# Kernel tuning notes

Hardware: AMD Instinct MI355X
Metric: run time of the kernel (lower is better)

The kernel has to match this reference:

```python
import jax, jax.numpy as jnp
import numpy as np

IN_F = 256
OUT_F = 256
H = 4
HD = OUT_F // H  # 64
N = 20000
E = 160000
B = 1
LN_EPS = 1e-5
NEG_SLOPE = 0.2


def setup_inputs() -> dict:
    key = jax.random.key(0)
    k1, k2, k3, k4 = jax.random.split(key, 4)
    node_features = jax.random.normal(k1, (B, N, IN_F), dtype=jnp.float32)
    edge_index = jax.random.randint(k2, (2, E), 0, N, dtype=jnp.int64)
    # per-head linear weights, stacked: [H, IN_F, HD]
    W = jax.random.normal(k3, (H, IN_F, HD), dtype=jnp.float32) / np.sqrt(IN_F)
    # per-head attention vectors on concat([src, dst]): [H, 2*HD]
    a = jax.random.normal(k4, (H, 2 * HD), dtype=jnp.float32) / np.sqrt(2 * HD)
    gamma = jnp.ones((OUT_F,), dtype=jnp.float32)
    beta = jnp.zeros((OUT_F,), dtype=jnp.float32)
    return {"node_features": node_features, "edge_index": edge_index,
            "W": W, "a": a, "gamma": gamma, "beta": beta}


def reference(node_features, edge_index, W, a, gamma, beta):
    src_idx, dst_idx = edge_index[0], edge_index[1]
    # per-head linear transform: [B, H, N, HD]
    t = jnp.einsum('bnf,hfd->bhnd', node_features, W)
    # gather edge endpoints: [B, H, E, HD]
    src = t[:, :, src_idx, :]
    dst = t[:, :, dst_idx, :]
    # attention score = a . concat(src, dst), split a into halves
    scores = (jnp.einsum('bhed,hd->bhe', src, a[:, :HD]) +
              jnp.einsum('bhed,hd->bhe', dst, a[:, HD:]))
    scores = jnp.where(scores >= 0, scores, NEG_SLOPE * scores)
    # NOTE: faithful to the original — softmax over ALL edges (dim=-1), not per-destination
    w = jax.nn.softmax(scores, axis=-1)  # [B, H, E]
    # scatter-add weighted src features into destination nodes
    agg = jnp.zeros_like(t).at[:, :, dst_idx, :].add(w[..., None] * src)  # [B, H, N, HD]
    # concat heads (head-major, matching torch.cat over head_outputs)
    out = agg.transpose(0, 2, 1, 3).reshape(B, N, OUT_F)
    # LayerNorm
    mean = out.mean(-1, keepdims=True)
    var = out.var(-1, keepdims=True)
    out = (out - mean) / jnp.sqrt(var + LN_EPS) * gamma + beta
    return out
```

## Files before the change

### kernel.cpp

```cpp
#include <hip/hip_runtime.h>

#define IN_F   256
#define OUT_F  256
#define NHEAD  4
#define HD     64
#define NN     20000
#define NE     160000
#define LN_EPS 1e-5f
#define SLOPE  0.2f
#define BUCKET 64
#define SE_BLOCKS 256

typedef __attribute__((ext_vector_type(8))) short short8;
typedef __attribute__((ext_vector_type(4))) float f32x4;

__device__ __forceinline__ unsigned short rne_bf16(float f) {
  unsigned u = __float_as_uint(f);
  u += 0x7FFFu + ((u >> 16) & 1u);
  return (unsigned short)(u >> 16);
}
__device__ __forceinline__ float bf2f(unsigned short u) {
  return __uint_as_float((unsigned)u << 16);
}
__device__ __forceinline__ unsigned pk2(float lo, float hi) {
  return (unsigned)rne_bf16(lo) | ((unsigned)rne_bf16(hi) << 16);
}

__global__ __launch_bounds__(256) void conv_w(const float* __restrict__ W,
                                              unsigned short* __restrict__ Wt,
                                              int* __restrict__ deg) {
  int i = blockIdx.x * 256 + threadIdx.x;
  if (i < NN) deg[i] = 0;
  if (i < 16384) {
    int fq  = i & 63;
    int col = i >> 6;
    int h = col >> 6, d = col & 63;
    const float* src = W + ((size_t)h * IN_F + fq * 4) * HD + d;
    ushort4 o;
    o.x = rne_bf16(src[0]);
    o.y = rne_bf16(src[64]);
    o.z = rne_bf16(src[128]);
    o.w = rne_bf16(src[192]);
    *reinterpret_cast<ushort4*>(Wt + (size_t)col * IN_F + fq * 4) = o;
  }
}

__global__ __launch_bounds__(256) void gemm_mfma(const float* __restrict__ X,
                                                 const unsigned short* __restrict__ Wt,
                                                 const float* __restrict__ a,
                                                 unsigned short* __restrict__ Tb,
                                                 float* __restrict__ asrc,
                                                 float* __restrict__ adst) {
  __shared__ unsigned Alds[64 * 32];
  __shared__ unsigned Blds[256 * 32];
  const int tid  = threadIdx.x;
  const int lane = tid & 63;
  const int wid  = tid >> 6;
  const int row0 = blockIdx.x * 64;

  f32x4 acc[4][4];
  #pragma unroll
  for (int r = 0; r < 4; ++r)
    #pragma unroll
    for (int c = 0; c < 4; ++c) acc[r][c] = (f32x4){0.f, 0.f, 0.f, 0.f};

  const int ar = tid >> 2;
  const int aq = tid & 3;
  const int s0 = (aq * 2) ^ (ar & 7);
  const int s1 = (aq * 2 + 1) ^ (ar & 7);
  const bool aok = (row0 + ar) < NN;
  const float* xrow = X + (size_t)(row0 + ar) * IN_F + aq * 16;

  for (int kt = 0; kt < 4; ++kt) {
    const int k0 = kt * 64;
    if (kt) __syncthreads();
    float4 x0 = {0,0,0,0}, x1 = {0,0,0,0}, x2 = {0,0,0,0}, x3 = {0,0,0,0};
    if (aok) {
      const float4* xp = reinterpret_cast<const float4*>(xrow + k0);
      x0 = xp[0]; x1 = xp[1]; x2 = xp[2]; x3 = xp[3];
    }
    uint4 U0 = {pk2(x0.x,x0.y), pk2(x0.z,x0.w), pk2(x1.x,x1.y), pk2(x1.z,x1.w)};
    uint4 U1 = {pk2(x2.x,x2.y), pk2(x2.z,x2.w), pk2(x3.x,x3.y), pk2(x3.z,x3.w)};
    *reinterpret_cast<uint4*>(&Alds[ar * 32 + s0 * 4]) = U0;
    *reinterpret_cast<uint4*>(&Alds[ar * 32 + s1 * 4]) = U1;
    #pragma unroll
    for (int i = 0; i < 8; ++i) {
      int c   = wid * 8 + i;
      int col = c * 8 + (lane >> 3);
      int kch = (lane & 7) ^ (col & 7);
      const unsigned short* src = Wt + (size_t)col * IN_F + k0 + kch * 8;
      __builtin_amdgcn_global_load_lds(
          (const __attribute__((address_space(1))) void*)src,
          (__attribute__((address_space(3))) void*)((char*)Blds + c * 1024),
          16, 0, 0);
    }
    __syncthreads();
    const int g = lane >> 4;
    #pragma unroll
    for (int kf = 0; kf < 2; ++kf) {
      short8 afr[4], bfr[4];
      #pragma unroll
      for (int r = 0; r < 4; ++r) {
        int row  = 16 * r + (lane & 15);
        int slot = (4 * kf + g) ^ (row & 7);
        afr[r] = *reinterpret_cast<const short8*>(&Alds[row * 32 + slot * 4]);
      }
      #pragma unroll
      for (int c = 0; c < 4; ++c) {
        int col  = wid * 64 + 16 * c + (lane & 15);
        int slot = (4 * kf + g) ^ (col & 7);
        bfr[c] = *reinterpret_cast<const short8*>(&Blds[col * 32 + slot * 4]);
      }
      #pragma unroll
      for (int r = 0; r < 4; ++r)
        #pragma unroll
        for (int c = 0; c < 4; ++c)
          acc[r][c] = __builtin_amdgcn_mfma_f32_16x16x32_bf16(afr[r], bfr[c], acc[r][c], 0, 0, 0);
    }
  }

  const int g  = lane >> 4;
  const int lc = lane & 15;
  float as_[4], ad_[4];
  #pragma unroll
  for (int fc = 0; fc < 4; ++fc) {
    as_[fc] = a[wid * 128 + fc * 16 + lc];
    ad_[fc] = a[wid * 128 + 64 + fc * 16 + lc];
  }
  #pragma unroll
  for (int r = 0; r < 4; ++r) {
    #pragma unroll
    for (int reg = 0; reg < 4; ++reg) {
      int row = row0 + 16 * r + g * 4 + reg;
      float ps = 0.f, pd = 0.f;
      if (row < NN) {
        #pragma unroll
        for (int fc = 0; fc < 4; ++fc) {
          float v = acc[r][fc][reg];
          ps = fmaf(v, as_[fc], ps);
          pd = fmaf(v, ad_[fc], pd);
          Tb[(size_t)row * OUT_F + wid * 64 + fc * 16 + lc] = rne_bf16(v);
        }
      }
      #pragma unroll
      for (int off = 1; off < 16; off <<= 1) {
        ps += __shfl_xor(ps, off, 64);
        pd += __shfl_xor(pd, off, 64);
      }
      if (lc == 0 && row < NN) {
        asrc[row * 4 + wid] = ps;
        adst[row * 4 + wid] = pd;
      }
    }
  }
}

__global__ __launch_bounds__(256) void score_exp_fill(const int* __restrict__ ei,
                                                      const float* __restrict__ asrc,
                                                      const float* __restrict__ adst,
                                                      float* __restrict__ partials,
                                                      int* __restrict__ deg,
                                                      int* __restrict__ srcs,
                                                      float4* __restrict__ wbuck) {
  __shared__ float red[4][4];
  const int tid  = threadIdx.x;
  const int lane = tid & 63;
  const int wid  = tid >> 6;
  float acc[4] = {0.f, 0.f, 0.f, 0.f};

  for (int e = blockIdx.x * 256 + tid; e < NE; e += SE_BLOCKS * 256) {
    int s = ei[e], t = ei[NE + e];
    float4 av = reinterpret_cast<const float4*>(asrc)[s];
    float4 dv = reinterpret_cast<const float4*>(adst)[t];
    float sc[4] = {av.x + dv.x, av.y + dv.y, av.z + dv.z, av.w + dv.w};
    float ex[4];
    #pragma unroll
    for (int h = 0; h < 4; ++h) {
      sc[h] = sc[h] >= 0.f ? sc[h] : SLOPE * sc[h];
      ex[h] = expf(sc[h]);
      acc[h] += ex[h];
    }
    int pos = atomicAdd(&deg[t], 1);
    srcs[t * BUCKET + pos]  = s;
    wbuck[t * BUCKET + pos] = make_float4(ex[0], ex[1], ex[2], ex[3]);
  }
  #pragma unroll
  for (int off = 1; off < 64; off <<= 1) {
    #pragma unroll
    for (int h = 0; h < 4; ++h) acc[h] += __shfl_xor(acc[h], off, 64);
  }
  if (lane == 0) {
    #pragma unroll
    for (int h = 0; h < 4; ++h) red[wid][h] = acc[h];
  }
  __syncthreads();
  if (tid < 4)
    partials[blockIdx.x * 4 + tid] = red[0][tid] + red[1][tid] + red[2][tid] + red[3][tid];
}

__global__ __launch_bounds__(256) void agg_ln_kernel(const int* __restrict__ deg,
                                                     const int* __restrict__ srcs,
                                                     const float* __restrict__ wbuck,
                                                     const float* __restrict__ partials,
                                                     const unsigned short* __restrict__ Tb,
                                                     const float* __restrict__ gamma,
                                                     const float* __restrict__ beta,
                                                     float* __restrict__ out) {
  __shared__ float red[256];
  const int tid  = threadIdx.x;
  const int lane = tid & 63;
  const int n    = blockIdx.x * 4 + (tid >> 6);
  const int h    = lane >> 4;

  float psum = partials[tid] + partials[tid + 256] + partials[tid + 512] + partials[tid + 768];

  int d = deg[n];
  const int*   bs = srcs  + (size_t)n * BUCKET;
  const float* bw = wbuck + (size_t)n * BUCKET * 4;
  const ushort4* T4 = reinterpret_cast<const ushort4*>(Tb);
  float4 acc = make_float4(0.f, 0.f, 0.f, 0.f);

  int p = 0;
  for (; p + 4 <= d; p += 4) {
    int s0 = bs[p], s1 = bs[p + 1], s2 = bs[p + 2], s3 = bs[p + 3];
    float w0 = bw[(p + 0) * 4 + h], w1 = bw[(p + 1) * 4 + h];
    float w2 = bw[(p + 2) * 4 + h], w3 = bw[(p + 3) * 4 + h];
    ushort4 v0 = T4[(size_t)s0 * 64 + lane];
    ushort4 v1 = T4[(size_t)s1 * 64 + lane];
    ushort4 v2 = T4[(size_t)s2 * 64 + lane];
    ushort4 v3 = T4[(size_t)s3 * 64 + lane];
    acc.x = fmaf(w3, bf2f(v3.x), fmaf(w2, bf2f(v2.x), fmaf(w1, bf2f(v1.x), fmaf(w0, bf2f(v0.x), acc.x))));
    acc.y = fmaf(w3, bf2f(v3.y), fmaf(w2, bf2f(v2.y), fmaf(w1, bf2f(v1.y), fmaf(w0, bf2f(v0.y), acc.y))));
    acc.z = fmaf(w3, bf2f(v3.z), fmaf(w2, bf2f(v2.z), fmaf(w1, bf2f(v1.z), fmaf(w0, bf2f(v0.z), acc.z))));
    acc.w = fmaf(w3, bf2f(v3.w), fmaf(w2, bf2f(v2.w), fmaf(w1, bf2f(v1.w), fmaf(w0, bf2f(v0.w), acc.w))));
  }
  for (; p < d; ++p) {
    int s0 = bs[p];
    float w0 = bw[p * 4 + h];
    ushort4 v0 = T4[(size_t)s0 * 64 + lane];
    acc.x = fmaf(w0, bf2f(v0.x), acc.x);
    acc.y = fmaf(w0, bf2f(v0.y), acc.y);
    acc.z = fmaf(w0, bf2f(v0.z), acc.z);
    acc.w = fmaf(w0, bf2f(v0.w), acc.w);
  }

  red[tid] = psum;
  __syncthreads();
  if (tid < 128) red[tid] += red[tid + 128];
  __syncthreads();
  if (tid < 64) red[tid] += red[tid + 64];
  __syncthreads();
  if (tid < 32) red[tid] += red[tid + 32];
  __syncthreads();
  if (tid < 16) red[tid] += red[tid + 16];
  __syncthreads();
  if (tid < 8) red[tid] += red[tid + 8];
  __syncthreads();
  if (tid < 4) red[tid] += red[tid + 4];
  __syncthreads();
  float rs = 1.0f / red[h];

  acc.x *= rs; acc.y *= rs; acc.z *= rs; acc.w *= rs;

  float s = acc.x + acc.y + acc.z + acc.w;
  float q = acc.x * acc.x + acc.y * acc.y + acc.z * acc.z + acc.w * acc.w;
  #pragma unroll
  for (int off = 1; off < 64; off <<= 1) {
    s += __shfl_xor(s, off, 64);
    q += __shfl_xor(q, off, 64);
  }
  float mean = s * (1.f / 256.f);
  float var  = q * (1.f / 256.f) - mean * mean;
  float rstd = rsqrtf(var + LN_EPS);
  float4 g = reinterpret_cast<const float4*>(gamma)[lane];
  float4 b = reinterpret_cast<const float4*>(beta)[lane];
  float4 o;
  o.x = (acc.x - mean) * rstd * g.x + b.x;
  o.y = (acc.y - mean) * rstd * g.y + b.y;
  o.z = (acc.z - mean) * rstd * g.z + b.z;
  o.w = (acc.w - mean) * rstd * g.w + b.w;
  reinterpret_cast<float4*>(out)[(size_t)n * 64 + lane] = o;
}

extern "C" void kernel_launch(void* const* d_in, const int* in_sizes, int n_in,
                              void* d_out, int out_size, void* d_ws, size_t ws_size,
                              hipStream_t stream) {
  const float* X     = (const float*)d_in[0];
  const int*   ei    = (const int*)d_in[1];
  const float* W     = (const float*)d_in[2];
  const float* a     = (const float*)d_in[3];
  const float* gamma = (const float*)d_in[4];
  const float* beta  = (const float*)d_in[5];
  float* out = (float*)d_out;

  float* ws = (float*)d_ws;
  const size_t OFF_DEG   = 16;
  const size_t OFF_PART  = OFF_DEG + NN;
  const size_t OFF_SRCS  = OFF_PART + 1024;
  const size_t OFF_WB    = OFF_SRCS + (size_t)NN * BUCKET;
  const size_t OFF_WT    = OFF_WB + (size_t)NN * BUCKET * 4;
  const size_t OFF_T     = OFF_WT + 32768;
  const size_t OFF_ASRC  = OFF_T + (size_t)NN * 128;
  const size_t OFF_ADST  = OFF_ASRC + NN * 4;

  int*            deg      = (int*)(ws + OFF_DEG);
  float*          partials = ws + OFF_PART;
  int*            srcs     = (int*)(ws + OFF_SRCS);
  float4*         wbuck    = (float4*)(ws + OFF_WB);
  unsigned short* Wt       = (unsigned short*)(ws + OFF_WT);
  unsigned short* Tb       = (unsigned short*)(ws + OFF_T);
  float*          asrc     = ws + OFF_ASRC;
  float*          adst     = ws + OFF_ADST;

  conv_w<<<80, 256, 0, stream>>>(W, Wt, deg);
  gemm_mfma<<<(NN + 63) / 64, 256, 0, stream>>>(X, Wt, a, Tb, asrc, adst);
  score_exp_fill<<<SE_BLOCKS, 256, 0, stream>>>(ei, asrc, adst, partials, deg, srcs,
                                                (float4*)wbuck);
  agg_ln_kernel<<<NN / 4, 256, 0, stream>>>(deg, srcs, (const float*)wbuck, partials,
                                            Tb, gamma, beta, out);
}
```

Baseline: 60.22 us.

## Pack edge buckets into int4 with bf16 weights and broadcast via shuffles

Merges the separate source-index and float4 weight buckets into one int4 record per edge, with the exp weights packed as bf16. The aggregation wave loads its whole bucket once (one slot per lane) and broadcasts source and weight with shuffles. Gathers are unrolled in chunks of 8/4/2/1 so more loads are in flight. This cuts bucket memory traffic and dependent scalar loads, at the cost of bf16 rounding on the attention weights and extra shuffle instructions.

```diff
diff --git a/kernel.cpp b/kernel.cpp
--- a/kernel.cpp
+++ b/kernel.cpp
@@ -160,8 +160,7 @@
                                                       const float* __restrict__ adst,
                                                       float* __restrict__ partials,
                                                       int* __restrict__ deg,
-                                                      int* __restrict__ srcs,
-                                                      float4* __restrict__ wbuck) {
+                                                      int4* __restrict__ bucket) {
   __shared__ float red[4][4];
   const int tid  = threadIdx.x;
   const int lane = tid & 63;
@@ -181,8 +180,8 @@
       acc[h] += ex[h];
     }
     int pos = atomicAdd(&deg[t], 1);
-    srcs[t * BUCKET + pos]  = s;
-    wbuck[t * BUCKET + pos] = make_float4(ex[0], ex[1], ex[2], ex[3]);
+    bucket[(size_t)t * BUCKET + pos] =
+        make_int4(s, (int)pk2(ex[0], ex[1]), (int)pk2(ex[2], ex[3]), 0);
   }
   #pragma unroll
   for (int off = 1; off < 64; off <<= 1) {
@@ -199,8 +198,7 @@
 }
 
 __global__ __launch_bounds__(256) void agg_ln_kernel(const int* __restrict__ deg,
-                                                     const int* __restrict__ srcs,
-                                                     const float* __restrict__ wbuck,
+                                                     const int4* __restrict__ bucket,
                                                      const float* __restrict__ partials,
                                                      const unsigned short* __restrict__ Tb,
                                                      const float* __restrict__ gamma,
@@ -215,34 +213,43 @@
   float psum = partials[tid] + partials[tid + 256] + partials[tid + 512] + partials[tid + 768];
 
   int d = deg[n];
-  const int*   bs = srcs  + (size_t)n * BUCKET;
-  const float* bw = wbuck + (size_t)n * BUCKET * 4;
+  int4 bv = bucket[(size_t)n * BUCKET + lane];
   const ushort4* T4 = reinterpret_cast<const ushort4*>(Tb);
   float4 acc = make_float4(0.f, 0.f, 0.f, 0.f);
 
+  #define SLOT_SW(pp, sv, wv)                                              \
+    {                                                                      \
+      sv = __shfl(bv.x, (pp), 64);                                         \
+      int _wl = __shfl(bv.y, (pp), 64);                                    \
+      int _wh = __shfl(bv.z, (pp), 64);                                    \
+      int _wd = (lane < 32) ? _wl : _wh;                                   \
+      wv = bf2f((unsigned short)((h & 1) ? ((unsigned)_wd >> 16)           \
+                                         : ((unsigned)_wd & 0xffffu)));    \
+    }
+  #define GATHER_CHUNK(CN)                                                 \
+    {                                                                      \
+      int sL[CN]; float wL[CN]; ushort4 vL[CN];                            \
+      _Pragma("unroll")                                                    \
+      for (int j = 0; j < CN; ++j) SLOT_SW(p + j, sL[j], wL[j]);           \
+      _Pragma("unroll")                                                    \
+      for (int j = 0; j < CN; ++j) vL[j] = T4[(size_t)sL[j] * 64 + lane];  \
+      _Pragma("unroll")                                                    \
+      for (int j = 0; j < CN; ++j) {                                       \
+        acc.x = fmaf(wL[j], bf2f(vL[j].x), acc.x);                         \
+        acc.y = fmaf(wL[j], bf2f(vL[j].y), acc.y);                         \
+        acc.z = fmaf(wL[j], bf2f(vL[j].z), acc.z);                         \
+        acc.w = fmaf(wL[j], bf2f(vL[j].w), acc.w);                         \
+      }                                                                    \
+      p += CN;                                                             \
+    }
+
   int p = 0;
-  for (; p + 4 <= d; p += 4) {
-    int s0 = bs[p], s1 = bs[p + 1], s2 = bs[p + 2], s3 = bs[p + 3];
-    float w0 = bw[(p + 0) * 4 + h], w1 = bw[(p + 1) * 4 + h];
-    float w2 = bw[(p + 2) * 4 + h], w3 = bw[(p + 3) * 4 + h];
-    ushort4 v0 = T4[(size_t)s0 * 64 + lane];
-    ushort4 v1 = T4[(size_t)s1 * 64 + lane];
-    ushort4 v2 = T4[(size_t)s2 * 64 + lane];
-    ushort4 v3 = T4[(size_t)s3 * 64 + lane];
-    acc.x = fmaf(w3, bf2f(v3.x), fmaf(w2, bf2f(v2.x), fmaf(w1, bf2f(v1.x), fmaf(w0, bf2f(v0.x), acc.x))));
-    acc.y = fmaf(w3, bf2f(v3.y), fmaf(w2, bf2f(v2.y), fmaf(w1, bf2f(v1.y), fmaf(w0, bf2f(v0.y), acc.y))));
-    acc.z = fmaf(w3, bf2f(v3.z), fmaf(w2, bf2f(v2.z), fmaf(w1, bf2f(v1.z), fmaf(w0, bf2f(v0.z), acc.z))));
-    acc.w = fmaf(w3, bf2f(v3.w), fmaf(w2, bf2f(v2.w), fmaf(w1, bf2f(v1.w), fmaf(w0, bf2f(v0.w), acc.w))));
-  }
-  for (; p < d; ++p) {
-    int s0 = bs[p];
-    float w0 = bw[p * 4 + h];
-    ushort4 v0 = T4[(size_t)s0 * 64 + lane];
-    acc.x = fmaf(w0, bf2f(v0.x), acc.x);
-    acc.y = fmaf(w0, bf2f(v0.y), acc.y);
-    acc.z = fmaf(w0, bf2f(v0.z), acc.z);
-    acc.w = fmaf(w0, bf2f(v0.w), acc.w);
-  }
+  while (p + 8 <= d) GATHER_CHUNK(8)
+  if (p + 4 <= d) GATHER_CHUNK(4)
+  if (p + 2 <= d) GATHER_CHUNK(2)
+  if (p < d)      GATHER_CHUNK(1)
+  #undef GATHER_CHUNK
+  #undef SLOT_SW
 
   red[tid] = psum;
   __syncthreads();
@@ -296,17 +303,15 @@
   float* ws = (float*)d_ws;
   const size_t OFF_DEG   = 16;
   const size_t OFF_PART  = OFF_DEG + NN;
-  const size_t OFF_SRCS  = OFF_PART + 1024;
-  const size_t OFF_WB    = OFF_SRCS + (size_t)NN * BUCKET;
-  const size_t OFF_WT    = OFF_WB + (size_t)NN * BUCKET * 4;
+  const size_t OFF_BUCK  = OFF_PART + 1024;
+  const size_t OFF_WT    = OFF_BUCK + (size_t)NN * BUCKET * 4;
   const size_t OFF_T     = OFF_WT + 32768;
   const size_t OFF_ASRC  = OFF_T + (size_t)NN * 128;
   const size_t OFF_ADST  = OFF_ASRC + NN * 4;
 
   int*            deg      = (int*)(ws + OFF_DEG);
   float*          partials = ws + OFF_PART;
-  int*            srcs     = (int*)(ws + OFF_SRCS);
-  float4*         wbuck    = (float4*)(ws + OFF_WB);
+  int4*           bucket   = (int4*)(ws + OFF_BUCK);
   unsigned short* Wt       = (unsigned short*)(ws + OFF_WT);
   unsigned short* Tb       = (unsigned short*)(ws + OFF_T);
   float*          asrc     = ws + OFF_ASRC;
@@ -314,8 +319,6 @@
 
   conv_w<<<80, 256, 0, stream>>>(W, Wt, deg);
   gemm_mfma<<<(NN + 63) / 64, 256, 0, stream>>>(X, Wt, a, Tb, asrc, adst);
-  score_exp_fill<<<SE_BLOCKS, 256, 0, stream>>>(ei, asrc, adst, partials, deg, srcs,
-                                                (float4*)wbuck);
-  agg_ln_kernel<<<NN / 4, 256, 0, stream>>>(deg, srcs, (const float*)wbuck, partials,
-                                            Tb, gamma, beta, out);
-}
+  score_exp_fill<<<SE_BLOCKS, 256, 0, stream>>>(ei, asrc, adst, partials, deg, bucket);
+  agg_ln_kernel<<<NN / 4, 256, 0, stream>>>(deg, bucket, partials, Tb, gamma, beta, out);
+}
```

New measurement: 58.57 us. 2.7% less time.
